# Optimization experiments

Measured on AMD Instinct MI355X. Metric: run time of the kernel, lower is better.

Reference implementation:

```python
import jax, jax.numpy as jnp
import numpy as np

ALPHA = 0.2  # LeakyReLU negative slope
MASK_FILL = -9e15


def setup_inputs() -> dict:
    key = jax.random.key(0)
    k_x, k_adj, k_W, k_a = jax.random.split(key, 4)
    B, N, Fin, T, O = 8, 1024, 64, 8, 128
    x = jax.random.normal(k_x, (B, N, Fin, T), dtype=jnp.float32)
    adj = (jax.random.uniform(k_adj, (N, N)) < 0.05).astype(jnp.float32)
    adj = jnp.maximum(adj, jnp.eye(N, dtype=jnp.float32))
    W = jax.random.normal(k_W, (Fin, O), dtype=jnp.float32) * (1.414 * (6.0 / (Fin + O)) ** 0.5)
    a = jax.random.normal(k_a, (2 * O, 1), dtype=jnp.float32) * (1.414 * (6.0 / (2 * O + 1)) ** 0.5)
    return {"x": x, "adj": adj, "W": W, "a": a}


def reference(x, adj, W, a):
    # x: (B, N, Fin, T), adj: (N, N), W: (Fin, O), a: (2O, 1)
    O = W.shape[1]
    xt = jnp.transpose(x, (0, 3, 1, 2))                 # (B, T, N, Fin)
    Wh = jnp.einsum('btnf,fo->btno', xt, W)             # (B, T, N, O)
    a1 = a[:O, 0]                                       # (O,)
    a2 = a[O:, 0]                                       # (O,)
    Wh1 = Wh @ a1                                       # (B, T, N)
    Wh2 = Wh @ a2                                       # (B, T, N)
    e = Wh1[..., :, None] + Wh2[..., None, :]           # (B, T, N, N): e_ij = Wh1_i + Wh2_j
    e = jax.nn.leaky_relu(e, negative_slope=ALPHA)
    e = jnp.where(adj > 0, e, MASK_FILL)
    attn = jax.nn.softmax(e, axis=-1)                   # softmax over neighbors j (torch dim=1 on (N,N))
    # dropout on attention is identity at inference (training=False)
    h_prime = jnp.einsum('btij,btjo->btio', attn, Wh)   # (B, T, N, O)
    out = jnp.transpose(h_prime, (0, 2, 3, 1))          # (B, N, O, T)
    return jax.nn.elu(out)                              # concat=True -> ELU
```

## Files before the change

### kernel.cpp

```cpp
#include <hip/hip_runtime.h>
#include <math.h>
#include <stdint.h>

#define ALPHA 0.2f

typedef __attribute__((ext_vector_type(8))) short bf16x8;
typedef __attribute__((ext_vector_type(4))) float f32x4;

__device__ __forceinline__ uint32_t pack_bf16(float a, float b) {
    return ((__float_as_uint(a) + 0x8000u) >> 16) |
           ((__float_as_uint(b) + 0x8000u) & 0xFFFF0000u);
}

__global__ __launch_bounds__(512) void k_wh(const float* __restrict__ x,
                                            const float* __restrict__ W,
                                            const float* __restrict__ a,
                                            uint4* __restrict__ Whf,
                                            float* __restrict__ Wh1,
                                            float* __restrict__ Wh2) {
    __shared__ float xs[16 * 512];
    __shared__ float Wv[128 * 68];

    const int tid = threadIdx.x;
    const int b   = blockIdx.x & 7;
    const int jt  = blockIdx.x >> 3;

    const float4* xg4 = (const float4*)(x + (size_t)(b * 1024 + jt * 16) * 512);
    #pragma unroll
    for (int i = 0; i < 4; ++i) {
        int    idx = tid + i * 512;
        float4 v   = xg4[idx];
        int jl  = idx >> 7;
        int rem = idx & 127;
        int f   = rem >> 1;
        int tq  = rem & 1;
        int kk  = f ^ ((jl >> 2) << 2);
        float* dst = &xs[jl * 512 + (tq * 4) * 64 + kk];
        dst[0]   = v.x;
        dst[64]  = v.y;
        dst[128] = v.z;
        dst[192] = v.w;
    }
    const float4* Wg4 = (const float4*)W;
    #pragma unroll
    for (int i = 0; i < 4; ++i) {
        int    idx = tid + i * 512;
        float4 v   = Wg4[idx];
        int k  = idx >> 5;
        int o0 = (idx & 31) * 4;
        #pragma unroll
        for (int c = 0; c < 4; ++c) {
            int o   = o0 + c;
            int adr = o * 68 + ((((k >> 2) ^ ((o >> 3) & 7)) << 2) | (k & 3));
            Wv[adr] = (&v.x)[c];
        }
    }
    __syncthreads();

    const int w  = tid >> 6;
    const int l  = tid & 63;
    const int q  = l >> 4;
    const int om = l & 15;
    const int t  = w;

    float acc[4][8];
    #pragma unroll
    for (int jj = 0; jj < 4; ++jj)
        #pragma unroll
        for (int nt = 0; nt < 8; ++nt) acc[jj][nt] = 0.f;

    for (int kc = 0; kc < 64; kc += 4) {
        float4 xv[4], wv[8];
        const int kx = kc ^ (q << 2);
        #pragma unroll
        for (int jj = 0; jj < 4; ++jj)
            xv[jj] = *(const float4*)&xs[(q * 4 + jj) * 512 + t * 64 + kx];
        #pragma unroll
        for (int nt = 0; nt < 8; ++nt) {
            int og  = nt * 16 + om;
            int grp = (kc >> 2) ^ ((nt * 2 + (om >> 3)) & 7);
            wv[nt]  = *(const float4*)&Wv[og * 68 + grp * 4];
        }
        #pragma unroll
        for (int jj = 0; jj < 4; ++jj) {
            #pragma unroll
            for (int nt = 0; nt < 8; ++nt) {
                float s = acc[jj][nt];
                s = fmaf(xv[jj].x, wv[nt].x, s);
                s = fmaf(xv[jj].y, wv[nt].y, s);
                s = fmaf(xv[jj].z, wv[nt].z, s);
                s = fmaf(xv[jj].w, wv[nt].w, s);
                acc[jj][nt] = s;
            }
        }
    }

    const int bt = b * 8 + t;

    float a1v[8], a2v[8];
    #pragma unroll
    for (int nt = 0; nt < 8; ++nt) {
        a1v[nt] = a[nt * 16 + om];
        a2v[nt] = a[128 + nt * 16 + om];
    }
    #pragma unroll
    for (int jj = 0; jj < 4; ++jj) {
        float s1 = 0.f, s2 = 0.f;
        #pragma unroll
        for (int nt = 0; nt < 8; ++nt) {
            s1 = fmaf(acc[jj][nt], a1v[nt], s1);
            s2 = fmaf(acc[jj][nt], a2v[nt], s2);
        }
        #pragma unroll
        for (int off = 1; off < 16; off <<= 1) {
            s1 += __shfl_xor(s1, off);
            s2 += __shfl_xor(s2, off);
        }
        if (om == 0) {
            int j = jt * 16 + q * 4 + jj;
            Wh1[bt * 1024 + j] = s1;
            Wh2[bt * 1024 + j] = s2;
        }
    }

    const int    q8l   = ((jt & 1) << 1) | (q >> 1);
    const int    l8    = (q8l << 4) | om;
    const size_t fbase = (size_t)(bt * 32 + (jt >> 1)) * 8;
    #pragma unroll
    for (int nt = 0; nt < 8; ++nt) {
        uint2 st;
        st.x = pack_bf16(acc[0][nt], acc[1][nt]);
        st.y = pack_bf16(acc[2][nt], acc[3][nt]);
        char* p = (char*)(Whf + (fbase + nt) * 64 + l8) + ((q & 1) << 3);
        *(uint2*)p = st;
    }
}

__global__ __launch_bounds__(256) void k_adjb(const float* __restrict__ adj,
                                              unsigned char* __restrict__ adjq) {
    int idx = blockIdx.x * 256 + threadIdx.x;
    int i   = idx >> 7;
    int pos = idx & 127;
    const float4* a4 = (const float4*)adj + idx * 2;
    float4 v0 = a4[0], v1 = a4[1];
    unsigned int by = 0;
    by |= (v0.x > 0.f) ? 1u : 0u;
    by |= (v0.y > 0.f) ? 2u : 0u;
    by |= (v0.z > 0.f) ? 4u : 0u;
    by |= (v0.w > 0.f) ? 8u : 0u;
    by |= (v1.x > 0.f) ? 16u : 0u;
    by |= (v1.y > 0.f) ? 32u : 0u;
    by |= (v1.z > 0.f) ? 64u : 0u;
    by |= (v1.w > 0.f) ? 128u : 0u;
    adjq[i * 128 + (pos & 3) * 32 + (pos >> 2)] = (unsigned char)by;
}

__global__ __launch_bounds__(512, 4) void k_agg(const uint4* __restrict__ Whf,
                                                const float* __restrict__ Wh1,
                                                const float* __restrict__ Wh2,
                                                const unsigned char* __restrict__ adjq,
                                                float* __restrict__ out) {
    __shared__ __attribute__((aligned(16))) uint4  bstage[2][512];
    __shared__ __attribute__((aligned(16))) float2 efs[1024];
    __shared__ float wh1s[128];
    __shared__ float m2s[8];

    const int tid   = threadIdx.x;
    const int b     = blockIdx.x & 7;
    const int t     = (blockIdx.x >> 3) & 7;
    const int itile = blockIdx.x >> 6;
    const int bt    = b * 8 + t;
    const int i0    = itile * 128;

    const int w = tid >> 6;
    const int l = tid & 63;
    const int q = l >> 4;
    const int m = l & 15;
    const int row = w * 16 + m;

    const uint4* plane = Whf + (size_t)bt * 16384;

    uint4 pf = plane[tid];
    const uint4* amask = (const uint4*)(adjq + (i0 + row) * 128 + q * 32);
    uint4 adj0 = amask[0];
    uint4 adj1 = amask[1];

    const float* wh2g = Wh2 + bt * 1024;
    float mx = -1e30f;
    #pragma unroll
    for (int rep = 0; rep < 2; ++rep) {
        int   j  = tid + rep * 512;
        float h2 = wh2g[j];
        float2 ef;
        ef.x = __expf(h2);
        ef.y = __expf(ALPHA * h2);
        efs[j] = ef;
        mx = fmaxf(mx, h2);
    }
    #pragma unroll
    for (int off = 1; off < 64; off <<= 1) mx = fmaxf(mx, __shfl_xor(mx, off));
    if (l == 0) m2s[w] = mx;
    if (tid < 128) wh1s[tid] = Wh1[bt * 1024 + i0 + tid];

    bstage[0][tid] = pf;
    __syncthreads();

    float M2 = m2s[0];
    #pragma unroll
    for (int i = 1; i < 8; ++i) M2 = fmaxf(M2, m2s[i]);

    const float h1 = wh1s[row];
    const float e0 = h1 + M2;
    const float mp = fmaxf(e0, ALPHA * e0);
    const float Af = __expf(h1 - mp);
    const float Bf = __expf(ALPHA * h1 - mp);
    const float G  = __expf(-h1);

    f32x4 acc[8];
    #pragma unroll
    for (int nt = 0; nt < 8; ++nt) acc[nt] = (f32x4){0.f, 0.f, 0.f, 0.f};
    f32x4 accl = (f32x4){0.f, 0.f, 0.f, 0.f};

    bf16x8 ones;
    #pragma unroll
    for (int i = 0; i < 8; ++i) ones[i] = (short)0x3F80;

    #pragma unroll
    for (int s = 0; s < 32; ++s) {
        if (s + 1 < 32) pf = plane[(s + 1) * 512 + tid];

        const float* eb = (const float*)&efs[s * 32 + q * 8];
        float4 ef01 = *(const float4*)(eb + 0);
        float4 ef23 = *(const float4*)(eb + 4);
        float4 ef45 = *(const float4*)(eb + 8);
        float4 ef67 = *(const float4*)(eb + 12);
        float E[8], F[8];
        E[0] = ef01.x; F[0] = ef01.y; E[1] = ef01.z; F[1] = ef01.w;
        E[2] = ef23.x; F[2] = ef23.y; E[3] = ef23.z; F[3] = ef23.w;
        E[4] = ef45.x; F[4] = ef45.y; E[5] = ef45.z; F[5] = ef45.w;
        E[6] = ef67.x; F[6] = ef67.y; E[7] = ef67.z; F[7] = ef67.w;

        const uint4   av = (s < 16) ? adj0 : adj1;
        const int     c  = (s >> 2) & 3;
        const uint32_t cw = (c == 0) ? av.x : (c == 1) ? av.y : (c == 2) ? av.z : av.w;
        const uint32_t by = (cw >> ((s & 3) * 8)) & 0xFFu;

        float p[8];
        #pragma unroll
        for (int jj = 0; jj < 8; ++jj) {
            bool  cond = E[jj] > G;
            float pr   = (cond ? Af : Bf) * (cond ? E[jj] : F[jj]);
            p[jj] = ((by >> jj) & 1u) ? pr : 0.0f;
        }
        union { uint32_t u[4]; bf16x8 v; } pk;
        #pragma unroll
        for (int pr2 = 0; pr2 < 4; ++pr2)
            pk.u[pr2] = pack_bf16(p[2 * pr2], p[2 * pr2 + 1]);

        const uint4* bp = &bstage[s & 1][l];
        #pragma unroll
        for (int nt = 0; nt < 8; ++nt) {
            union { uint4 u; bf16x8 v; } br;
            br.u = bp[nt * 64];
            acc[nt] = __builtin_amdgcn_mfma_f32_16x16x32_bf16(pk.v, br.v, acc[nt], 0, 0, 0);
        }
        accl = __builtin_amdgcn_mfma_f32_16x16x32_bf16(pk.v, ones, accl, 0, 0, 0);

        if (s + 1 < 32) bstage[(s + 1) & 1][tid] = pf;
        __syncthreads();
    }

    float* og = out + ((size_t)(b * 1024 + i0 + w * 16)) * 1024 + t;
    #pragma unroll
    for (int reg = 0; reg < 4; ++reg) {
        const int   r    = q * 4 + reg;
        const float linv = 1.0f / accl[reg];
        #pragma unroll
        for (int nt = 0; nt < 8; ++nt) {
            float v = acc[nt][reg] * linv;
            v = v > 0.f ? v : __expf(v) - 1.f;
            og[(size_t)r * 1024 + (nt * 16 + m) * 8] = v;
        }
    }
}

extern "C" void kernel_launch(void* const* d_in, const int* in_sizes, int n_in,
                              void* d_out, int out_size, void* d_ws, size_t ws_size,
                              hipStream_t stream) {
    const float* x   = (const float*)d_in[0];
    const float* adj = (const float*)d_in[1];
    const float* W   = (const float*)d_in[2];
    const float* a   = (const float*)d_in[3];
    float* out = (float*)d_out;

    uint4*         Whf  = (uint4*)d_ws;
    float*         Wh1  = (float*)(Whf + 1048576);
    float*         Wh2  = Wh1 + 65536;
    unsigned char* adjq = (unsigned char*)(Wh2 + 65536);

    k_wh  <<<512, 512, 0, stream>>>(x, W, a, Whf, Wh1, Wh2);
    k_adjb<<<512, 256, 0, stream>>>(adj, adjq);
    k_agg <<<512, 512, 0, stream>>>(Whf, Wh1, Wh2, adjq, out);
}
```

Before: 147.3 us.

## Switch aggregation to 32x32x16 MFMA tiles with packed bf16 exp table

The aggregation kernel moves from 16x16x32 to 32x32x16 bf16 MFMA. Each wave now owns 32 rows, blocks shrink to 256 threads, and each thread stages 4 B fragments per step over 16 double-buffered iterations. The Whf and adjacency-bitmask layouts produced by the earlier kernels are rewritten to match the new fragment ordering. The per-column exp(h2) and exp(alpha*h2) table is packed as bf16 pairs to halve LDS traffic. The aim is fewer MFMA issues, LDS reads and barriers per unit of work, at the cost of bf16 rounding of the exponent factors and more registers per thread.

```diff
diff --git a/kernel.cpp b/kernel.cpp
--- a/kernel.cpp
+++ b/kernel.cpp
@@ -4,8 +4,9 @@
 
 #define ALPHA 0.2f
 
-typedef __attribute__((ext_vector_type(8))) short bf16x8;
-typedef __attribute__((ext_vector_type(4))) float f32x4;
+typedef __attribute__((ext_vector_type(8)))  short bf16x8;
+typedef __attribute__((ext_vector_type(4)))  float f32x4;
+typedef __attribute__((ext_vector_type(16))) float f32x16;
 
 __device__ __forceinline__ uint32_t pack_bf16(float a, float b) {
     return ((__float_as_uint(a) + 0x8000u) >> 16) |
@@ -123,15 +124,14 @@
         }
     }
 
-    const int    q8l   = ((jt & 1) << 1) | (q >> 1);
-    const int    l8    = (q8l << 4) | om;
-    const size_t fbase = (size_t)(bt * 32 + (jt >> 1)) * 8;
     #pragma unroll
     for (int nt = 0; nt < 8; ++nt) {
         uint2 st;
         st.x = pack_bf16(acc[0][nt], acc[1][nt]);
         st.y = pack_bf16(acc[2][nt], acc[3][nt]);
-        char* p = (char*)(Whf + (fbase + nt) * 64 + l8) + ((q & 1) << 3);
+        int    lane2 = ((q >> 1) << 5) | ((nt & 1) << 4) | om;
+        size_t fidx  = ((size_t)(bt * 4 + (nt >> 1)) * 64 + jt) * 64 + lane2;
+        char*  p     = (char*)(Whf + fidx) + ((q & 1) << 3);
         *(uint2*)p = st;
     }
 }
@@ -152,18 +152,18 @@
     by |= (v1.y > 0.f) ? 32u : 0u;
     by |= (v1.z > 0.f) ? 64u : 0u;
     by |= (v1.w > 0.f) ? 128u : 0u;
-    adjq[i * 128 + (pos & 3) * 32 + (pos >> 2)] = (unsigned char)by;
-}
-
-__global__ __launch_bounds__(512, 4) void k_agg(const uint4* __restrict__ Whf,
-                                                const float* __restrict__ Wh1,
-                                                const float* __restrict__ Wh2,
-                                                const unsigned char* __restrict__ adjq,
-                                                float* __restrict__ out) {
-    __shared__ __attribute__((aligned(16))) uint4  bstage[2][512];
-    __shared__ __attribute__((aligned(16))) float2 efs[1024];
+    adjq[(i << 7) + ((pos & 1) << 6) + (((pos >> 1) & 1) << 5) + (pos >> 2)] = (unsigned char)by;
+}
+
+__global__ __launch_bounds__(256) void k_agg(const uint4* __restrict__ Whf,
+                                             const float* __restrict__ Wh1,
+                                             const float* __restrict__ Wh2,
+                                             const unsigned char* __restrict__ adjq,
+                                             float* __restrict__ out) {
+    __shared__ __attribute__((aligned(16))) uint4    bstage[2][1024];
+    __shared__ __attribute__((aligned(16))) uint32_t efs[1024];
     __shared__ float wh1s[128];
-    __shared__ float m2s[8];
+    __shared__ float m2s[4];
 
     const int tid   = threadIdx.x;
     const int b     = blockIdx.x & 7;
@@ -172,29 +172,34 @@
     const int bt    = b * 8 + t;
     const int i0    = itile * 128;
 
-    const int w = tid >> 6;
-    const int l = tid & 63;
-    const int q = l >> 4;
-    const int m = l & 15;
-    const int row = w * 16 + m;
+    const int w   = tid >> 6;
+    const int l   = tid & 63;
+    const int col = l & 31;
+    const int g   = l >> 5;
+    const int row = w * 32 + col;
 
     const uint4* plane = Whf + (size_t)bt * 16384;
-
-    uint4 pf = plane[tid];
-    const uint4* amask = (const uint4*)(adjq + (i0 + row) * 128 + q * 32);
-    uint4 adj0 = amask[0];
-    uint4 adj1 = amask[1];
+    const int    c     = w;
+    const int    li    = l;
+
+    uint4 pf[4];
+    #pragma unroll
+    for (int f = 0; f < 4; ++f) pf[f] = plane[(c * 64 + f) * 64 + li];
+
+    const uint4* ap = (const uint4*)(adjq + ((size_t)(i0 + row) << 7) + (g << 6));
+    uint4 am[4];
+    #pragma unroll
+    for (int f = 0; f < 4; ++f) am[f] = ap[f];
 
     const float* wh2g = Wh2 + bt * 1024;
     float mx = -1e30f;
     #pragma unroll
-    for (int rep = 0; rep < 2; ++rep) {
-        int   j  = tid + rep * 512;
+    for (int rep = 0; rep < 4; ++rep) {
+        int   j  = tid + rep * 256;
         float h2 = wh2g[j];
-        float2 ef;
-        ef.x = __expf(h2);
-        ef.y = __expf(ALPHA * h2);
-        efs[j] = ef;
+        float E  = __expf(h2);
+        float F  = __expf(ALPHA * h2);
+        efs[j] = pack_bf16(E, F);
         mx = fmaxf(mx, h2);
     }
     #pragma unroll
@@ -202,13 +207,11 @@
     if (l == 0) m2s[w] = mx;
     if (tid < 128) wh1s[tid] = Wh1[bt * 1024 + i0 + tid];
 
-    bstage[0][tid] = pf;
+    #pragma unroll
+    for (int f = 0; f < 4; ++f) bstage[0][(c * 4 + f) * 64 + li] = pf[f];
     __syncthreads();
 
-    float M2 = m2s[0];
-    #pragma unroll
-    for (int i = 1; i < 8; ++i) M2 = fmaxf(M2, m2s[i]);
-
+    const float M2 = fmaxf(fmaxf(m2s[0], m2s[1]), fmaxf(m2s[2], m2s[3]));
     const float h1 = wh1s[row];
     const float e0 = h1 + M2;
     const float mp = fmaxf(e0, ALPHA * e0);
@@ -216,70 +219,89 @@
     const float Bf = __expf(ALPHA * h1 - mp);
     const float G  = __expf(-h1);
 
-    f32x4 acc[8];
-    #pragma unroll
-    for (int nt = 0; nt < 8; ++nt) acc[nt] = (f32x4){0.f, 0.f, 0.f, 0.f};
-    f32x4 accl = (f32x4){0.f, 0.f, 0.f, 0.f};
+    f32x16 acc[4];
+    #pragma unroll
+    for (int nt2 = 0; nt2 < 4; ++nt2)
+        #pragma unroll
+        for (int r = 0; r < 16; ++r) acc[nt2][r] = 0.f;
+    f32x16 accl;
+    #pragma unroll
+    for (int r = 0; r < 16; ++r) accl[r] = 0.f;
 
     bf16x8 ones;
     #pragma unroll
     for (int i = 0; i < 8; ++i) ones[i] = (short)0x3F80;
 
     #pragma unroll
-    for (int s = 0; s < 32; ++s) {
-        if (s + 1 < 32) pf = plane[(s + 1) * 512 + tid];
-
-        const float* eb = (const float*)&efs[s * 32 + q * 8];
-        float4 ef01 = *(const float4*)(eb + 0);
-        float4 ef23 = *(const float4*)(eb + 4);
-        float4 ef45 = *(const float4*)(eb + 8);
-        float4 ef67 = *(const float4*)(eb + 12);
-        float E[8], F[8];
-        E[0] = ef01.x; F[0] = ef01.y; E[1] = ef01.z; F[1] = ef01.w;
-        E[2] = ef23.x; F[2] = ef23.y; E[3] = ef23.z; F[3] = ef23.w;
-        E[4] = ef45.x; F[4] = ef45.y; E[5] = ef45.z; F[5] = ef45.w;
-        E[6] = ef67.x; F[6] = ef67.y; E[7] = ef67.z; F[7] = ef67.w;
-
-        const uint4   av = (s < 16) ? adj0 : adj1;
-        const int     c  = (s >> 2) & 3;
-        const uint32_t cw = (c == 0) ? av.x : (c == 1) ? av.y : (c == 2) ? av.z : av.w;
-        const uint32_t by = (cw >> ((s & 3) * 8)) & 0xFFu;
-
-        float p[8];
-        #pragma unroll
-        for (int jj = 0; jj < 8; ++jj) {
-            bool  cond = E[jj] > G;
-            float pr   = (cond ? Af : Bf) * (cond ? E[jj] : F[jj]);
-            p[jj] = ((by >> jj) & 1u) ? pr : 0.0f;
-        }
-        union { uint32_t u[4]; bf16x8 v; } pk;
-        #pragma unroll
-        for (int pr2 = 0; pr2 < 4; ++pr2)
-            pk.u[pr2] = pack_bf16(p[2 * pr2], p[2 * pr2 + 1]);
-
-        const uint4* bp = &bstage[s & 1][l];
-        #pragma unroll
-        for (int nt = 0; nt < 8; ++nt) {
-            union { uint4 u; bf16x8 v; } br;
-            br.u = bp[nt * 64];
-            acc[nt] = __builtin_amdgcn_mfma_f32_16x16x32_bf16(pk.v, br.v, acc[nt], 0, 0, 0);
-        }
-        accl = __builtin_amdgcn_mfma_f32_16x16x32_bf16(pk.v, ones, accl, 0, 0, 0);
-
-        if (s + 1 < 32) bstage[(s + 1) & 1][tid] = pf;
+    for (int u = 0; u < 16; ++u) {
+        if (u + 1 < 16) {
+            #pragma unroll
+            for (int f = 0; f < 4; ++f)
+                pf[f] = plane[(c * 64 + (u + 1) * 4 + f) * 64 + li];
+        }
+
+        #pragma unroll
+        for (int d = 0; d < 2; ++d) {
+            const int s = u * 2 + d;
+            #pragma unroll
+            for (int h = 0; h < 2; ++h) {
+                const int jb = s * 32 + h * 16 + g * 8;
+                uint4 efa = *(const uint4*)&efs[jb];
+                uint4 efb = *(const uint4*)&efs[jb + 4];
+                uint32_t ef[8] = {efa.x, efa.y, efa.z, efa.w,
+                                  efb.x, efb.y, efb.z, efb.w};
+
+                const int      pe = h * 32 + s;
+                const uint4    av = am[pe >> 4];
+                const int      cc = (pe >> 2) & 3;
+                const uint32_t cw = (cc == 0) ? av.x : (cc == 1) ? av.y
+                                   : (cc == 2) ? av.z : av.w;
+                const uint32_t by = (cw >> ((pe & 3) * 8)) & 0xFFu;
+
+                float p[8];
+                #pragma unroll
+                for (int e = 0; e < 8; ++e) {
+                    float E  = __uint_as_float(ef[e] << 16);
+                    float F  = __uint_as_float(ef[e] & 0xFFFF0000u);
+                    bool  cd = E > G;
+                    float pr = (cd ? Af : Bf) * (cd ? E : F);
+                    p[e] = ((by >> e) & 1u) ? pr : 0.0f;
+                }
+                union { uint32_t u32[4]; bf16x8 v; } pk;
+                #pragma unroll
+                for (int r = 0; r < 4; ++r)
+                    pk.u32[r] = pack_bf16(p[2 * r], p[2 * r + 1]);
+
+                #pragma unroll
+                for (int nt2 = 0; nt2 < 4; ++nt2) {
+                    union { uint4 u4; bf16x8 v; } br;
+                    br.u4 = bstage[u & 1][(nt2 * 4 + d * 2 + h) * 64 + l];
+                    acc[nt2] = __builtin_amdgcn_mfma_f32_32x32x16_bf16(
+                        pk.v, br.v, acc[nt2], 0, 0, 0);
+                }
+                accl = __builtin_amdgcn_mfma_f32_32x32x16_bf16(
+                    pk.v, ones, accl, 0, 0, 0);
+            }
+        }
+
+        if (u + 1 < 16) {
+            #pragma unroll
+            for (int f = 0; f < 4; ++f)
+                bstage[(u + 1) & 1][(c * 4 + f) * 64 + li] = pf[f];
+        }
         __syncthreads();
     }
 
-    float* og = out + ((size_t)(b * 1024 + i0 + w * 16)) * 1024 + t;
-    #pragma unroll
-    for (int reg = 0; reg < 4; ++reg) {
-        const int   r    = q * 4 + reg;
+    float* og = out + ((size_t)(b * 1024 + i0 + w * 32)) * 1024 + t;
+    #pragma unroll
+    for (int reg = 0; reg < 16; ++reg) {
+        const int   r    = (reg & 3) + 8 * (reg >> 2) + 4 * g;
         const float linv = 1.0f / accl[reg];
         #pragma unroll
-        for (int nt = 0; nt < 8; ++nt) {
-            float v = acc[nt][reg] * linv;
+        for (int nt2 = 0; nt2 < 4; ++nt2) {
+            float v = acc[nt2][reg] * linv;
             v = v > 0.f ? v : __expf(v) - 1.f;
-            og[(size_t)r * 1024 + (nt * 16 + m) * 8] = v;
+            og[(size_t)r * 1024 + (nt2 * 32 + col) * 8] = v;
         }
     }
 }
@@ -300,5 +322,5 @@
 
     k_wh  <<<512, 512, 0, stream>>>(x, W, a, Whf, Wh1, Wh2);
     k_adjb<<<512, 256, 0, stream>>>(adj, adjq);
-    k_agg <<<512, 512, 0, stream>>>(Whf, Wh1, Wh2, adjq, out);
-}
+    k_agg <<<512, 256, 0, stream>>>(Whf, Wh1, Wh2, adjq, out);
+}
```

New measurement: 150.4 us. 2.1% more time.
